# Kernel optimization log

Hardware: AMD Instinct MI355X
Metric: run time of the kernel (lower is better)

## Reference

```python
import jax, jax.numpy as jnp
import numpy as np

N_NODES = 50000
N_EDGES = 800000
FEAT = 64
N_LAYERS = 3


def setup_inputs() -> dict:
    key = jax.random.key(0)
    ks = jax.random.split(key, 6)
    x = jax.random.normal(ks[0], (N_NODES, FEAT), dtype=jnp.float32)
    edge_index = jax.random.randint(ks[1], (2, N_EDGES), 0, N_NODES, dtype=jnp.int64)
    s = 1.0 / np.sqrt(2 * FEAT)
    W1 = jax.random.uniform(ks[2], (N_LAYERS, 2 * FEAT, FEAT), jnp.float32, -s, s)
    b1 = jax.random.uniform(ks[3], (N_LAYERS, FEAT), jnp.float32, -s, s)
    s2 = 1.0 / np.sqrt(FEAT)
    W2 = jax.random.uniform(ks[4], (N_LAYERS, FEAT, FEAT), jnp.float32, -s2, s2)
    b2 = jax.random.uniform(ks[5], (N_LAYERS, FEAT), jnp.float32, -s2, s2)
    return {"x": x, "edge_index": edge_index, "W1": W1, "b1": b1, "W2": W2, "b2": b2}


def _edgeconv(x, src, dst, W1, b1, W2, b2):
    # PyG EdgeConv: message = mlp([x_i, x_j - x_i]), aggr = max over incoming edges
    xi = x[dst]                                  # [E, F] target features
    xj = x[src]                                  # [E, F] source features
    m = jnp.concatenate([xi, xj - xi], axis=-1)  # [E, 2F]
    h = jax.nn.relu(m @ W1 + b1)                 # [E, F]
    h = h @ W2 + b2                              # [E, F]
    out = jax.ops.segment_max(h, dst, num_segments=x.shape[0])
    # isolated nodes: -inf -> 0 (matches torch_scatter max fill)
    return jnp.where(jnp.isfinite(out), out, 0.0)


def reference(x, edge_index, W1, b1, W2, b2):
    src, dst = edge_index[0], edge_index[1]
    for l in range(N_LAYERS):
        x = _edgeconv(x, src, dst, W1[l], b1[l], W2[l], b2[l])
        x = jax.nn.relu(x)
    return x
```

## Files before the change

kernel.cpp:

```cpp
#include <hip/hip_runtime.h>

#define NN 50000
#define NE 800000
#define F  64
#define NBKT 196
#define CHUNK (NE / 256)

typedef __attribute__((ext_vector_type(8))) short bf16x8;
typedef __attribute__((ext_vector_type(4))) float f32x4;

#define WS_FLAG   0u
#define WS_WCTH   256u
#define WS_WCTL   49408u
#define WS_W2TH   98560u
#define WS_W2TL   123136u
#define WS_SEDGE  147712u
#define WS_U      3347712u
#define WS_V      16147712u
#define WS_BHT    (WS_U + 0u)
#define WS_BOT    (WS_U + 200960u)
#define WS_CSUM   (WS_U + 401920u)
#define WS_BASE   (WS_U + 402944u)
#define WS_TMP    (WS_V + 0u)

__device__ __forceinline__ float relu_f(float a) { return a > 0.f ? a : 0.f; }

__device__ __forceinline__ void pack4(float f0, float f1, float f2, float f3,
                                      unsigned& hw0, unsigned& hw1,
                                      unsigned& lw0, unsigned& lw1) {
    unsigned u0 = __float_as_uint(f0), u1 = __float_as_uint(f1);
    unsigned u2 = __float_as_uint(f2), u3 = __float_as_uint(f3);
    unsigned h0 = u0 & 0xffff0000u, h1 = u1 & 0xffff0000u;
    unsigned h2 = u2 & 0xffff0000u, h3 = u3 & 0xffff0000u;
    float l0 = f0 - __uint_as_float(h0), l1 = f1 - __uint_as_float(h1);
    float l2 = f2 - __uint_as_float(h2), l3 = f3 - __uint_as_float(h3);
    hw0 = h1 | (h0 >> 16);
    hw1 = h3 | (h2 >> 16);
    lw0 = (__float_as_uint(l1) & 0xffff0000u) | (__float_as_uint(l0) >> 16);
    lw1 = (__float_as_uint(l3) & 0xffff0000u) | (__float_as_uint(l2) >> 16);
}

__global__ void detect_kernel(const int* __restrict__ idx, int* __restrict__ flag) {
    int t = blockIdx.x * blockDim.x + threadIdx.x;
    if (idx[2 * t + 1] != 0) atomicOr(flag, 1);
}

__global__ void prep_kernel(const float* __restrict__ W1, const float* __restrict__ W2,
                            unsigned short* __restrict__ WCTH, unsigned short* __restrict__ WCTL,
                            unsigned short* __restrict__ W2TH, unsigned short* __restrict__ W2TL) {
    int i = blockIdx.x * blockDim.x + threadIdx.x;
    int l = i >> 12;
    int r = i & 4095;
    int k = r >> 6;
    int j = r & 63;
    float wa = W1[l * 8192 + k * 64 + j];
    float wb = W1[l * 8192 + 4096 + k * 64 + j];
    float a = wa - wb;
    unsigned ua = __float_as_uint(a), ahi = ua & 0xffff0000u;
    float alo = a - __uint_as_float(ahi);
    WCTH[l * 8192 + j * 64 + k] = (unsigned short)(ahi >> 16);
    WCTL[l * 8192 + j * 64 + k] = (unsigned short)(__float_as_uint(alo) >> 16);
    unsigned ub = __float_as_uint(wb), bhi = ub & 0xffff0000u;
    float blo = wb - __uint_as_float(bhi);
    WCTH[l * 8192 + (64 + j) * 64 + k] = (unsigned short)(bhi >> 16);
    WCTL[l * 8192 + (64 + j) * 64 + k] = (unsigned short)(__float_as_uint(blo) >> 16);
    float w = W2[l * 4096 + k * 64 + j];
    unsigned uw = __float_as_uint(w), whi = uw & 0xffff0000u;
    float wlo = w - __uint_as_float(whi);
    W2TH[l * 4096 + j * 64 + k] = (unsigned short)(whi >> 16);
    W2TL[l * 4096 + j * 64 + k] = (unsigned short)(__float_as_uint(wlo) >> 16);
}

__global__ __launch_bounds__(256, 2) void gemm_mfma(
    const float* __restrict__ xin,
    const unsigned short* __restrict__ WCTH, const unsigned short* __restrict__ WCTL,
    const float* __restrict__ b1,
    float* __restrict__ U, float* __restrict__ V) {
    __shared__ char smem[65536];
    int lane = threadIdx.x & 63;
    int wib  = threadIdx.x >> 6;
    char* base = smem + wib * 16384;
    char* Hhi = base;
    char* Hlo = base + 8192;
    int l15 = lane & 15, l4 = lane >> 4;

    int wid = blockIdx.x * 4 + wib;
    int b = wid >> 1;
    int half = wid & 1;

    bf16x8 Bh[2][4], Bl[2][4];
#pragma unroll
    for (int kt = 0; kt < 2; ++kt)
#pragma unroll
        for (int nt = 0; nt < 4; ++nt) {
            int off = (half * 64 + nt * 16 + l15) * 64 + kt * 32 + l4 * 8;
            Bh[kt][nt] = *(const bf16x8*)(WCTH + off);
            Bl[kt][nt] = *(const bf16x8*)(WCTL + off);
        }

    int jj = lane & 15;
    int rsub = lane >> 4;
#pragma unroll
    for (int i = 0; i < 16; ++i) {
        int r = 4 * i + rsub;
        int node = b * 64 + r;
        int cnode = node < NN ? node : NN - 1;
        float4 xv = *(const float4*)(xin + (size_t)cnode * F + 4 * jj);
        unsigned hw0, hw1, lw0, lw1;
        pack4(xv.x, xv.y, xv.z, xv.w, hw0, hw1, lw0, lw1);
        int g = jj >> 1;
        int byt = r * 128 + ((g ^ (r & 7)) << 4) + (jj & 1) * 8;
        *(uint2*)(Hhi + byt) = make_uint2(hw0, hw1);
        *(uint2*)(Hlo + byt) = make_uint2(lw0, lw1);
    }

    f32x4 acc[4][4];
#pragma unroll
    for (int mt = 0; mt < 4; ++mt)
#pragma unroll
        for (int nt = 0; nt < 4; ++nt)
            acc[mt][nt] = (f32x4){0.f, 0.f, 0.f, 0.f};
#pragma unroll
    for (int mt = 0; mt < 4; ++mt) {
        int arow = mt * 16 + l15;
        int abase = arow * 128;
        int am = arow & 7;
        bf16x8 Ah0 = *(const bf16x8*)(Hhi + abase + (((0 + l4) ^ am) << 4));
        bf16x8 Ah1 = *(const bf16x8*)(Hhi + abase + (((4 + l4) ^ am) << 4));
        bf16x8 Al0 = *(const bf16x8*)(Hlo + abase + (((0 + l4) ^ am) << 4));
        bf16x8 Al1 = *(const bf16x8*)(Hlo + abase + (((4 + l4) ^ am) << 4));
#pragma unroll
        for (int nt = 0; nt < 4; ++nt) {
            f32x4 a = acc[mt][nt];
            a = __builtin_amdgcn_mfma_f32_16x16x32_bf16(Ah0, Bh[0][nt], a, 0, 0, 0);
            a = __builtin_amdgcn_mfma_f32_16x16x32_bf16(Ah1, Bh[1][nt], a, 0, 0, 0);
            a = __builtin_amdgcn_mfma_f32_16x16x32_bf16(Al0, Bh[0][nt], a, 0, 0, 0);
            a = __builtin_amdgcn_mfma_f32_16x16x32_bf16(Al1, Bh[1][nt], a, 0, 0, 0);
            a = __builtin_amdgcn_mfma_f32_16x16x32_bf16(Ah0, Bl[0][nt], a, 0, 0, 0);
            a = __builtin_amdgcn_mfma_f32_16x16x32_bf16(Ah1, Bl[1][nt], a, 0, 0, 0);
            acc[mt][nt] = a;
        }
    }

    float bc[4];
#pragma unroll
    for (int nt = 0; nt < 4; ++nt)
        bc[nt] = (half == 0) ? b1[nt * 16 + l15] : 0.f;
    float* outp = (half == 0) ? U : V;
#pragma unroll
    for (int mt = 0; mt < 4; ++mt)
#pragma unroll
        for (int nt = 0; nt < 4; ++nt) {
            int col = nt * 16 + l15;
#pragma unroll
            for (int r = 0; r < 4; ++r) {
                int row = b * 64 + mt * 16 + l4 * 4 + r;
                if (row < NN) outp[(size_t)row * F + col] = acc[mt][nt][r] + bc[nt];
            }
        }
}

__global__ __launch_bounds__(256) void histA_kernel(const int* __restrict__ idx,
                                                    const int* __restrict__ flag,
                                                    int* __restrict__ bhistT) {
    __shared__ int h[NBKT];
    int tid = threadIdx.x, blk = blockIdx.x;
    if (tid < NBKT) h[tid] = 0;
    __syncthreads();
    int fl = *flag;
    int start = blk * CHUNK;
    for (int i = tid; i < CHUNK; i += 256) {
        int e = start + i;
        int dst = fl ? idx[NE + e] : idx[2 * NE + 2 * e];
        atomicAdd(&h[dst >> 8], 1);
    }
    __syncthreads();
    if (tid < NBKT) bhistT[tid * 256 + blk] = h[tid];
}

__global__ __launch_bounds__(256) void scanCols_kernel(const int* __restrict__ bhistT,
                                                       int* __restrict__ boffT,
                                                       int* __restrict__ csum) {
    __shared__ int buf[256];
    int t = threadIdx.x, b = blockIdx.x;
    int v = bhistT[b * 256 + t];
    buf[t] = v;
    __syncthreads();
    for (int d = 1; d < 256; d <<= 1) {
        int add = (t >= d) ? buf[t - d] : 0;
        __syncthreads();
        buf[t] += add;
        __syncthreads();
    }
    boffT[b * 256 + t] = buf[t] - v;
    if (t == 255) csum[b] = buf[255];
}

__global__ __launch_bounds__(256) void scanBase_kernel(const int* __restrict__ csum,
                                                       int* __restrict__ base) {
    __shared__ int buf[256];
    int t = threadIdx.x;
    int v = (t < NBKT) ? csum[t] : 0;
    buf[t] = v;
    __syncthreads();
    for (int d = 1; d < 256; d <<= 1) {
        int add = (t >= d) ? buf[t - d] : 0;
        __syncthreads();
        buf[t] += add;
        __syncthreads();
    }
    if (t < NBKT) base[t] = buf[t] - v;
}

__global__ __launch_bounds__(256) void scatterA2_kernel(const int* __restrict__ idx,
                                                        const int* __restrict__ flag,
                                                        const int* __restrict__ boffT,
                                                        const int* __restrict__ base,
                                                        unsigned* __restrict__ tmp) {
    __shared__ int loc[NBKT];
    __shared__ int bb[NBKT];
    int tid = threadIdx.x, blk = blockIdx.x;
    if (tid < NBKT) { loc[tid] = 0; bb[tid] = base[tid] + boffT[tid * 256 + blk]; }
    __syncthreads();
    int fl = *flag;
    int start = blk * CHUNK;
    for (int i = tid; i < CHUNK; i += 256) {
        int e = start + i;
        int src, dst;
        if (fl) { src = idx[e];     dst = idx[NE + e]; }
        else    { src = idx[2 * e]; dst = idx[2 * NE + 2 * e]; }
        int bkt = dst >> 8;
        int my = atomicAdd(&loc[bkt], 1);
        tmp[bb[bkt] + my] = ((unsigned)dst << 16) | (unsigned)src;
    }
}

__global__ __launch_bounds__(256) void sortC_kernel(const unsigned* __restrict__ tmp,
                                                    const int* __restrict__ base,
                                                    const int* __restrict__ csum,
                                                    unsigned* __restrict__ sedge) {
    __shared__ int cnt[256];
    __shared__ int pos[256];
    int b = blockIdx.x, t = threadIdx.x;
    int start = base[b], n = csum[b];
    cnt[t] = 0;
    __syncthreads();
    for (int i = t; i < n; i += 256)
        atomicAdd(&cnt[(tmp[start + i] >> 16) & 255], 1);
    __syncthreads();
    int v = cnt[t];
    pos[t] = v;
    __syncthreads();
    for (int d = 1; d < 256; d <<= 1) {
        int add = (t >= d) ? pos[t - d] : 0;
        __syncthreads();
        pos[t] += add;
        __syncthreads();
    }
    int excl = pos[t] - v;
    __syncthreads();
    pos[t] = excl;
    __syncthreads();
    for (int i = t; i < n; i += 256) {
        unsigned w = tmp[start + i];
        int p = atomicAdd(&pos[(w >> 16) & 255], 1);
        sedge[start + p] = w;
    }
}

__global__ __launch_bounds__(256, 2) void edge_kernel(
    const unsigned* __restrict__ sedge,
    const float* __restrict__ U, const float* __restrict__ V,
    const unsigned short* __restrict__ W2TH, const unsigned short* __restrict__ W2TL,
    const float* __restrict__ b2, float* __restrict__ out) {
    __shared__ char smem[65536];
    int lane = threadIdx.x & 63;
    int wib  = threadIdx.x >> 6;
    char* base = smem + wib * 16384;
    char* Hhi = base;
    char* Hlo = base + 8192;
    float* segA = (float*)Hhi;
    float* segB = (float*)Hlo;
    unsigned* edlds = (unsigned*)Hhi;
    int l15 = lane & 15, l4 = lane >> 4;

    float bias = b2[lane];

    bf16x8 Bh[2][4], Bl[2][4];
#pragma unroll
    for (int kt = 0; kt < 2; ++kt)
#pragma unroll
        for (int nt = 0; nt < 4; ++nt) {
            int off = (nt * 16 + l15) * 64 + kt * 32 + l4 * 8;
            Bh[kt][nt] = *(const bf16x8*)(W2TH + off);
            Bl[kt][nt] = *(const bf16x8*)(W2TL + off);
        }

    int bid = blockIdx.x;
    int swz = (bid & 7) * 64 + (bid >> 3);
    int wid = swz * 4 + wib;
    const int NB = NE / 64;
    int bstart = (int)(((long long)wid * NB) >> 11);
    int bend   = (int)(((long long)(wid + 1) * NB) >> 11);

    float run = -3.402823e38f;
    int   segdst = -1;
    bool  firstflush = true;

    int jj = lane & 15;
    int rsub = lane >> 4;

    for (int b = bstart; b < bend; ++b) {
        int e = b * 64 + lane;
        unsigned pe = sedge[e];
        int dst = (int)(pe >> 16);

        edlds[lane] = pe;
        unsigned pr[16];
#pragma unroll
        for (int q = 0; q < 16; ++q) pr[q] = edlds[4 * q + rsub];

#pragma unroll
        for (int h = 0; h < 2; ++h) {
            float4 uu[8], vv[8];
#pragma unroll
            for (int q = 0; q < 8; ++q) {
                unsigned p = pr[8 * h + q];
                int sr = (int)(p & 0xffffu);
                int dr = (int)(p >> 16);
                uu[q] = *(const float4*)(U + (size_t)dr * F + 4 * jj);
                vv[q] = *(const float4*)(V + (size_t)sr * F + 4 * jj);
            }
#pragma unroll
            for (int q = 0; q < 8; ++q) {
                int r = 32 * h + 4 * q + rsub;
                float4 ua = uu[q], va = vv[q];
                unsigned hw0, hw1, lw0, lw1;
                pack4(relu_f(ua.x + va.x), relu_f(ua.y + va.y),
                      relu_f(ua.z + va.z), relu_f(ua.w + va.w), hw0, hw1, lw0, lw1);
                int g = jj >> 1;
                int byt = r * 128 + ((g ^ (r & 7)) << 4) + (jj & 1) * 8;
                *(uint2*)(Hhi + byt) = make_uint2(hw0, hw1);
                *(uint2*)(Hlo + byt) = make_uint2(lw0, lw1);
            }
        }

        int pdst = __shfl_up(dst, 1, 64);
        bool leader = (lane == 0) || (pdst != dst);
        unsigned long long lead_mask = __ballot(leader);
        unsigned leadlo = (unsigned)lead_mask;
        unsigned leadhi = (unsigned)(lead_mask >> 32);
        int contB = (leadhi & 1u) ? 0 : 1;

        f32x4 acc[4][4];
#pragma unroll
        for (int mt = 0; mt < 4; ++mt)
#pragma unroll
            for (int nt = 0; nt < 4; ++nt)
                acc[mt][nt] = (f32x4){0.f, 0.f, 0.f, 0.f};
#pragma unroll
        for (int mt = 0; mt < 4; ++mt) {
            int arow = mt * 16 + l15;
            int abase = arow * 128;
            int am = arow & 7;
            bf16x8 Ah0 = *(const bf16x8*)(Hhi + abase + (((0 + l4) ^ am) << 4));
            bf16x8 Ah1 = *(const bf16x8*)(Hhi + abase + (((4 + l4) ^ am) << 4));
            bf16x8 Al0 = *(const bf16x8*)(Hlo + abase + (((0 + l4) ^ am) << 4));
            bf16x8 Al1 = *(const bf16x8*)(Hlo + abase + (((4 + l4) ^ am) << 4));
#pragma unroll
            for (int nt = 0; nt < 4; ++nt) {
                f32x4 a = acc[mt][nt];
                a = __builtin_amdgcn_mfma_f32_16x16x32_bf16(Ah0, Bh[0][nt], a, 0, 0, 0);
                a = __builtin_amdgcn_mfma_f32_16x16x32_bf16(Ah1, Bh[1][nt], a, 0, 0, 0);
                a = __builtin_amdgcn_mfma_f32_16x16x32_bf16(Al0, Bh[0][nt], a, 0, 0, 0);
                a = __builtin_amdgcn_mfma_f32_16x16x32_bf16(Al1, Bh[1][nt], a, 0, 0, 0);
                a = __builtin_amdgcn_mfma_f32_16x16x32_bf16(Ah0, Bl[0][nt], a, 0, 0, 0);
                a = __builtin_amdgcn_mfma_f32_16x16x32_bf16(Ah1, Bl[1][nt], a, 0, 0, 0);
                acc[mt][nt] = a;
            }
        }

        int usedA = __popc(leadlo);
        int usedB = __popc(leadhi) + contB;
        for (int s = 0; s < usedA; ++s) segA[s * 64 + lane] = -3.402823e38f;
        for (int s = 0; s < usedB; ++s) segB[s * 64 + lane] = -3.402823e38f;

        int sid[4][4];
#pragma unroll
        for (int mt = 0; mt < 4; ++mt)
#pragma unroll
            for (int r = 0; r < 4; ++r) {
                int row = mt * 16 + l4 * 4 + r;
                sid[mt][r] = (row < 32)
                    ? __popc(leadlo & ((2u << row) - 1u)) - 1
                    : __popc(leadhi & ((2u << (row - 32)) - 1u)) - 1 + contB;
            }

#pragma unroll
        for (int mt = 0; mt < 4; ++mt)
#pragma unroll
            for (int nt = 0; nt < 4; ++nt)
#pragma unroll
                for (int r = 0; r < 4; ++r) {
                    float* sb = (mt < 2) ? segA : segB;
                    (void)__hip_atomic_fetch_max(
                        &sb[sid[mt][r] * 64 + nt * 16 + l15], acc[mt][nt][r],
                        __ATOMIC_RELAXED, __HIP_MEMORY_SCOPE_WAVEFRONT);
                }

        unsigned mA = leadlo;
        for (int s = 0; s < usedA; ++s) {
            int rb = __ffs(mA) - 1; mA &= mA - 1u;
            int dsts = __shfl(dst, rb, 64);
            float val = segA[s * 64 + lane];
            if (dsts != segdst) {
                if (segdst >= 0) {
                    float v = fmaxf(run + bias, 0.f);
                    if (firstflush) {
                        if (v > 0.f)
                            atomicMax((int*)(out + (size_t)segdst * F + lane),
                                      __float_as_int(v));
                        firstflush = false;
                    } else {
                        out[(size_t)segdst * F + lane] = v;
                    }
                }
                segdst = dsts; run = val;
            } else run = fmaxf(run, val);
        }
        int dst32 = __shfl(dst, 32, 64);
        unsigned mB = leadhi;
        for (int s = 0; s < usedB; ++s) {
            int dsts;
            if (s == 0 && contB) dsts = dst32;
            else { int rb = __ffs(mB) - 1; mB &= mB - 1u; dsts = __shfl(dst, 32 + rb, 64); }
            float val = segB[s * 64 + lane];
            if (dsts != segdst) {
                if (segdst >= 0) {
                    float v = fmaxf(run + bias, 0.f);
                    if (firstflush) {
                        if (v > 0.f)
                            atomicMax((int*)(out + (size_t)segdst * F + lane),
                                      __float_as_int(v));
                        firstflush = false;
                    } else {
                        out[(size_t)segdst * F + lane] = v;
                    }
                }
                segdst = dsts; run = val;
            } else run = fmaxf(run, val);
        }
    }
    if (segdst >= 0) {
        float val = fmaxf(run + bias, 0.f);
        if (val > 0.f)
            atomicMax((int*)(out + (size_t)segdst * F + lane), __float_as_int(val));
    }
}

extern "C" void kernel_launch(void* const* d_in, const int* in_sizes, int n_in,
                              void* d_out, int out_size, void* d_ws, size_t ws_size,
                              hipStream_t stream) {
    const float* x  = (const float*)d_in[0];
    const int*   ei = (const int*)d_in[1];
    const float* W1 = (const float*)d_in[2];
    const float* b1 = (const float*)d_in[3];
    const float* W2 = (const float*)d_in[4];
    const float* b2 = (const float*)d_in[5];
    float* out = (float*)d_out;

    char* ws = (char*)d_ws;
    int*            flag   = (int*)(ws + WS_FLAG);
    unsigned short* WCTH   = (unsigned short*)(ws + WS_WCTH);
    unsigned short* WCTL   = (unsigned short*)(ws + WS_WCTL);
    unsigned short* W2TH   = (unsigned short*)(ws + WS_W2TH);
    unsigned short* W2TL   = (unsigned short*)(ws + WS_W2TL);
    unsigned*       sedge  = (unsigned*)(ws + WS_SEDGE);
    float*          Ubuf   = (float*)(ws + WS_U);
    float*          Vbuf   = (float*)(ws + WS_V);
    int*            bhistT = (int*)(ws + WS_BHT);
    int*            boffT  = (int*)(ws + WS_BOT);
    int*            csum   = (int*)(ws + WS_CSUM);
    int*            baseb  = (int*)(ws + WS_BASE);
    unsigned*       tmp    = (unsigned*)(ws + WS_TMP);

    hipMemsetAsync(flag, 0, 4, stream);
    detect_kernel<<<16, 256, 0, stream>>>(ei, flag);
    prep_kernel<<<48, 256, 0, stream>>>(W1, W2, WCTH, WCTL, W2TH, W2TL);
    histA_kernel<<<256, 256, 0, stream>>>(ei, flag, bhistT);
    scanCols_kernel<<<NBKT, 256, 0, stream>>>(bhistT, boffT, csum);
    scanBase_kernel<<<1, 256, 0, stream>>>(csum, baseb);
    scatterA2_kernel<<<256, 256, 0, stream>>>(ei, flag, boffT, baseb, tmp);
    sortC_kernel<<<NBKT, 256, 0, stream>>>(tmp, baseb, csum, sedge);

    const float* xin = x;
    for (int l = 0; l < 3; ++l) {
        gemm_mfma<<<391, 256, 0, stream>>>(xin, WCTH + l * 8192, WCTL + l * 8192,
                                           b1 + l * 64, Ubuf, Vbuf);
        hipMemsetAsync(out, 0, (size_t)NN * F * sizeof(float), stream);
        edge_kernel<<<512, 256, 0, stream>>>(sedge, Ubuf, Vbuf,
                                             W2TH + l * 4096, W2TL + l * 4096,
                                             b2 + l * 64, out);
        xin = out;
    }
}
```

Baseline: 250.5 us.

## Prefetch next block's V rows into LDS with async global-to-LDS loads

The edge kernel now prefetches the next 64-edge block's source-node V rows straight into LDS with global_load_lds, issued after the MFMA stage, and double-buffers the edge indices in LDS. The segment-max scratch shrinks to an 8-segment window processed in chunks, which cuts LDS per wave to about 18.5 KB. Blocks drop to 2 waves (1024 blocks of 128 threads) so more waves fit per CU. The aim is to hide gather latency behind compute and raise occupancy, at the cost of a full vmcnt(0) wait each iteration and a chunked loop over segments.

```diff
diff --git a/kernel.cpp b/kernel.cpp
--- a/kernel.cpp
+++ b/kernel.cpp
@@ -39,6 +39,14 @@
     lw0 = (__float_as_uint(l1) & 0xffff0000u) | (__float_as_uint(l0) >> 16);
     lw1 = (__float_as_uint(l3) & 0xffff0000u) | (__float_as_uint(l2) >> 16);
 }
+
+__device__ __forceinline__ void glds16(const float* g, void* l) {
+    __builtin_amdgcn_global_load_lds(
+        (const __attribute__((address_space(1))) unsigned*)g,
+        (__attribute__((address_space(3))) unsigned*)l, 16, 0, 0);
+}
+
+__device__ __forceinline__ int permJ(int j) { return (j >= 4 && j < 12) ? (j ^ 12) : j; }
 
 __global__ void detect_kernel(const int* __restrict__ idx, int* __restrict__ flag) {
     int t = blockIdx.x * blockDim.x + threadIdx.x;
@@ -268,21 +276,20 @@
     }
 }
 
-__global__ __launch_bounds__(256, 2) void edge_kernel(
+#define WSTR 18944
+__global__ __launch_bounds__(128, 2) void edge_kernel(
     const unsigned* __restrict__ sedge,
     const float* __restrict__ U, const float* __restrict__ V,
     const unsigned short* __restrict__ W2TH, const unsigned short* __restrict__ W2TL,
     const float* __restrict__ b2, float* __restrict__ out) {
-    __shared__ char smem[65536];
+    __shared__ char smem[2 * WSTR];
     int lane = threadIdx.x & 63;
     int wib  = threadIdx.x >> 6;
-    char* base = smem + wib * 16384;
-    char* Hhi = base;
-    char* Hlo = base + 8192;
-    float* segA = (float*)Hhi;
-    float* segB = (float*)Hlo;
-    unsigned* edlds = (unsigned*)Hhi;
+    char* R = smem + wib * WSTR;
+    float* seg = (float*)(R + 16384);
+    unsigned* ebuf = (unsigned*)(R + 18432);
     int l15 = lane & 15, l4 = lane >> 4;
+    int jj = lane & 15, rsub = lane >> 4;
 
     float bias = b2[lane];
 
@@ -297,60 +304,75 @@
         }
 
     int bid = blockIdx.x;
-    int swz = (bid & 7) * 64 + (bid >> 3);
-    int wid = swz * 4 + wib;
+    int swz = (bid & 7) * 128 + (bid >> 3);
+    int wid = swz * 2 + wib;
     const int NB = NE / 64;
     int bstart = (int)(((long long)wid * NB) >> 11);
     int bend   = (int)(((long long)(wid + 1) * NB) >> 11);
+    if (bstart >= bend) return;
 
     float run = -3.402823e38f;
     int   segdst = -1;
     bool  firstflush = true;
 
-    int jj = lane & 15;
-    int rsub = lane >> 4;
+    unsigned pe = sedge[bstart * 64 + lane];
+    ebuf[(bstart & 1) * 64 + lane] = pe;
+    {
+        const unsigned* ebn = ebuf + (bstart & 1) * 64;
+#pragma unroll
+        for (int k = 0; k < 16; ++k) {
+            int pk = permJ(k);
+            unsigned ew = ebn[4 * pk + l4];
+            int sr = (int)(ew & 0xffffu);
+            glds16(V + (size_t)sr * F + 4 * jj, R + k * 1024);
+        }
+    }
 
     for (int b = bstart; b < bend; ++b) {
-        int e = b * 64 + lane;
-        unsigned pe = sedge[e];
+        int par = b & 1;
+        const unsigned* eb = ebuf + par * 64;
+
+        unsigned pe_n = 0;
+        if (b + 1 < bend) pe_n = sedge[(b + 1) * 64 + lane];
+
+        asm volatile("s_waitcnt vmcnt(0)" ::: "memory");
+        __builtin_amdgcn_sched_barrier(0);
+
         int dst = (int)(pe >> 16);
 
-        edlds[lane] = pe;
-        unsigned pr[16];
-#pragma unroll
-        for (int q = 0; q < 16; ++q) pr[q] = edlds[4 * q + rsub];
-
 #pragma unroll
         for (int h = 0; h < 2; ++h) {
-            float4 uu[8], vv[8];
+            float4 vvr[8], uu[8];
 #pragma unroll
             for (int q = 0; q < 8; ++q) {
-                unsigned p = pr[8 * h + q];
-                int sr = (int)(p & 0xffffu);
-                int dr = (int)(p >> 16);
+                int j = 8 * h + q;
+                int k = permJ(j);
+                vvr[q] = *(const float4*)(R + k * 1024 + rsub * 256 + jj * 16);
+            }
+#pragma unroll
+            for (int q = 0; q < 8; ++q) {
+                int row = 32 * h + 4 * q + rsub;
+                unsigned ew = eb[row];
+                int dr = (int)(ew >> 16);
                 uu[q] = *(const float4*)(U + (size_t)dr * F + 4 * jj);
-                vv[q] = *(const float4*)(V + (size_t)sr * F + 4 * jj);
             }
 #pragma unroll
             for (int q = 0; q < 8; ++q) {
                 int r = 32 * h + 4 * q + rsub;
-                float4 ua = uu[q], va = vv[q];
+                float4 ua = uu[q], va = vvr[q];
                 unsigned hw0, hw1, lw0, lw1;
                 pack4(relu_f(ua.x + va.x), relu_f(ua.y + va.y),
                       relu_f(ua.z + va.z), relu_f(ua.w + va.w), hw0, hw1, lw0, lw1);
                 int g = jj >> 1;
                 int byt = r * 128 + ((g ^ (r & 7)) << 4) + (jj & 1) * 8;
-                *(uint2*)(Hhi + byt) = make_uint2(hw0, hw1);
-                *(uint2*)(Hlo + byt) = make_uint2(lw0, lw1);
+                *(uint2*)(R + byt) = make_uint2(hw0, hw1);
+                *(uint2*)(R + 8192 + byt) = make_uint2(lw0, lw1);
             }
         }
 
         int pdst = __shfl_up(dst, 1, 64);
         bool leader = (lane == 0) || (pdst != dst);
-        unsigned long long lead_mask = __ballot(leader);
-        unsigned leadlo = (unsigned)lead_mask;
-        unsigned leadhi = (unsigned)(lead_mask >> 32);
-        int contB = (leadhi & 1u) ? 0 : 1;
+        unsigned long long lead = __ballot(leader);
 
         f32x4 acc[4][4];
 #pragma unroll
@@ -363,10 +385,10 @@
             int arow = mt * 16 + l15;
             int abase = arow * 128;
             int am = arow & 7;
-            bf16x8 Ah0 = *(const bf16x8*)(Hhi + abase + (((0 + l4) ^ am) << 4));
-            bf16x8 Ah1 = *(const bf16x8*)(Hhi + abase + (((4 + l4) ^ am) << 4));
-            bf16x8 Al0 = *(const bf16x8*)(Hlo + abase + (((0 + l4) ^ am) << 4));
-            bf16x8 Al1 = *(const bf16x8*)(Hlo + abase + (((4 + l4) ^ am) << 4));
+            bf16x8 Ah0 = *(const bf16x8*)(R + abase + (((0 + l4) ^ am) << 4));
+            bf16x8 Ah1 = *(const bf16x8*)(R + abase + (((4 + l4) ^ am) << 4));
+            bf16x8 Al0 = *(const bf16x8*)(R + 8192 + abase + (((0 + l4) ^ am) << 4));
+            bf16x8 Al1 = *(const bf16x8*)(R + 8192 + abase + (((4 + l4) ^ am) << 4));
 #pragma unroll
             for (int nt = 0; nt < 4; ++nt) {
                 f32x4 a = acc[mt][nt];
@@ -380,76 +402,67 @@
             }
         }
 
-        int usedA = __popc(leadlo);
-        int usedB = __popc(leadhi) + contB;
-        for (int s = 0; s < usedA; ++s) segA[s * 64 + lane] = -3.402823e38f;
-        for (int s = 0; s < usedB; ++s) segB[s * 64 + lane] = -3.402823e38f;
-
+        __builtin_amdgcn_sched_barrier(0);
+        if (b + 1 < bend) {
+            ebuf[(par ^ 1) * 64 + lane] = pe_n;
+            const unsigned* ebn = ebuf + (par ^ 1) * 64;
+#pragma unroll
+            for (int k = 0; k < 16; ++k) {
+                int pk = permJ(k);
+                unsigned ew = ebn[4 * pk + l4];
+                int sr = (int)(ew & 0xffffu);
+                glds16(V + (size_t)sr * F + 4 * jj, R + k * 1024);
+            }
+        }
+
+        int used = __popcll(lead);
         int sid[4][4];
 #pragma unroll
         for (int mt = 0; mt < 4; ++mt)
 #pragma unroll
             for (int r = 0; r < 4; ++r) {
                 int row = mt * 16 + l4 * 4 + r;
-                sid[mt][r] = (row < 32)
-                    ? __popc(leadlo & ((2u << row) - 1u)) - 1
-                    : __popc(leadhi & ((2u << (row - 32)) - 1u)) - 1 + contB;
-            }
-
-#pragma unroll
-        for (int mt = 0; mt < 4; ++mt)
-#pragma unroll
-            for (int nt = 0; nt < 4; ++nt)
-#pragma unroll
-                for (int r = 0; r < 4; ++r) {
-                    float* sb = (mt < 2) ? segA : segB;
-                    (void)__hip_atomic_fetch_max(
-                        &sb[sid[mt][r] * 64 + nt * 16 + l15], acc[mt][nt][r],
-                        __ATOMIC_RELAXED, __HIP_MEMORY_SCOPE_WAVEFRONT);
-                }
-
-        unsigned mA = leadlo;
-        for (int s = 0; s < usedA; ++s) {
-            int rb = __ffs(mA) - 1; mA &= mA - 1u;
-            int dsts = __shfl(dst, rb, 64);
-            float val = segA[s * 64 + lane];
-            if (dsts != segdst) {
-                if (segdst >= 0) {
-                    float v = fmaxf(run + bias, 0.f);
-                    if (firstflush) {
-                        if (v > 0.f)
-                            atomicMax((int*)(out + (size_t)segdst * F + lane),
-                                      __float_as_int(v));
-                        firstflush = false;
-                    } else {
-                        out[(size_t)segdst * F + lane] = v;
+                sid[mt][r] = __popcll(lead & ((2ull << row) - 1ull)) - 1;
+            }
+
+        unsigned long long mwalk = lead;
+        for (int sb = 0; sb < used; sb += 8) {
+            int ns = used - sb; if (ns > 8) ns = 8;
+            for (int s = 0; s < ns; ++s) seg[s * 64 + lane] = -3.402823e38f;
+#pragma unroll
+            for (int mt = 0; mt < 4; ++mt)
+#pragma unroll
+                for (int nt = 0; nt < 4; ++nt)
+#pragma unroll
+                    for (int r = 0; r < 4; ++r) {
+                        int t = sid[mt][r] - sb;
+                        if ((unsigned)t < 8u)
+                            (void)__hip_atomic_fetch_max(
+                                &seg[t * 64 + nt * 16 + l15], acc[mt][nt][r],
+                                __ATOMIC_RELAXED, __HIP_MEMORY_SCOPE_WAVEFRONT);
                     }
-                }
-                segdst = dsts; run = val;
-            } else run = fmaxf(run, val);
-        }
-        int dst32 = __shfl(dst, 32, 64);
-        unsigned mB = leadhi;
-        for (int s = 0; s < usedB; ++s) {
-            int dsts;
-            if (s == 0 && contB) dsts = dst32;
-            else { int rb = __ffs(mB) - 1; mB &= mB - 1u; dsts = __shfl(dst, 32 + rb, 64); }
-            float val = segB[s * 64 + lane];
-            if (dsts != segdst) {
-                if (segdst >= 0) {
-                    float v = fmaxf(run + bias, 0.f);
-                    if (firstflush) {
-                        if (v > 0.f)
-                            atomicMax((int*)(out + (size_t)segdst * F + lane),
-                                      __float_as_int(v));
-                        firstflush = false;
-                    } else {
-                        out[(size_t)segdst * F + lane] = v;
+            for (int s = 0; s < ns; ++s) {
+                int rb = __ffsll((long long)mwalk) - 1; mwalk &= mwalk - 1ull;
+                int dsts = __shfl(dst, rb, 64);
+                float val = seg[s * 64 + lane];
+                if (dsts != segdst) {
+                    if (segdst >= 0) {
+                        float v = fmaxf(run + bias, 0.f);
+                        if (firstflush) {
+                            if (v > 0.f)
+                                atomicMax((int*)(out + (size_t)segdst * F + lane),
+                                          __float_as_int(v));
+                            firstflush = false;
+                        } else {
+                            out[(size_t)segdst * F + lane] = v;
+                        }
                     }
-                }
-                segdst = dsts; run = val;
-            } else run = fmaxf(run, val);
-        }
+                    segdst = dsts; run = val;
+                } else run = fmaxf(run, val);
+            }
+        }
+
+        pe = pe_n;
     }
     if (segdst >= 0) {
         float val = fmaxf(run + bias, 0.f);
@@ -498,9 +511,9 @@
         gemm_mfma<<<391, 256, 0, stream>>>(xin, WCTH + l * 8192, WCTL + l * 8192,
                                            b1 + l * 64, Ubuf, Vbuf);
         hipMemsetAsync(out, 0, (size_t)NN * F * sizeof(float), stream);
-        edge_kernel<<<512, 256, 0, stream>>>(sedge, Ubuf, Vbuf,
-                                             W2TH + l * 4096, W2TL + l * 4096,
-                                             b2 + l * 64, out);
+        edge_kernel<<<1024, 128, 0, stream>>>(sedge, Ubuf, Vbuf,
+                                              W2TH + l * 4096, W2TL + l * 4096,
+                                              b2 + l * 64, out);
         xin = out;
     }
 }
```

New measurement: 286.7 us. 1.14x slower.
